# Kernel tuning notes

Measured on AMD Instinct MI355X. Metric: run time of the kernel, lower is better.

Reference implementation:

```python
import jax, jax.numpy as jnp
import numpy as np

N_EMBED = 1024
NUM_HEADS = 16
HEAD_SIZE = 64  # NUM_HEADS * HEAD_SIZE == N_EMBED
BLOCK_SIZE = 2048


def setup_inputs() -> dict:
    key = jax.random.key(0)
    ks = jax.random.split(key, 9)
    s = 1.0 / np.sqrt(N_EMBED)
    batch_x = jax.random.normal(ks[0], (4, BLOCK_SIZE, N_EMBED), dtype=jnp.float32)
    # stacked per-head linear params: weight [H, E, d], bias [H, d]
    Wq = jax.random.uniform(ks[1], (NUM_HEADS, N_EMBED, HEAD_SIZE), jnp.float32, -s, s)
    Wk = jax.random.uniform(ks[2], (NUM_HEADS, N_EMBED, HEAD_SIZE), jnp.float32, -s, s)
    Wv = jax.random.uniform(ks[3], (NUM_HEADS, N_EMBED, HEAD_SIZE), jnp.float32, -s, s)
    bq = jax.random.uniform(ks[4], (NUM_HEADS, HEAD_SIZE), jnp.float32, -s, s)
    bk = jax.random.uniform(ks[5], (NUM_HEADS, HEAD_SIZE), jnp.float32, -s, s)
    bv = jax.random.uniform(ks[6], (NUM_HEADS, HEAD_SIZE), jnp.float32, -s, s)
    Wp = jax.random.uniform(ks[7], (N_EMBED, N_EMBED), jnp.float32, -s, s)
    bp = jax.random.uniform(ks[8], (N_EMBED,), jnp.float32, -s, s)
    return {"batch_x": batch_x, "Wq": Wq, "Wk": Wk, "Wv": Wv,
            "bq": bq, "bk": bk, "bv": bv, "Wp": Wp, "bp": bp}


def reference(batch_x, Wq, Wk, Wv, bq, bk, bv, Wp, bp):
    B, T, E = batch_x.shape
    # per-head projections: [B, H, T, d]
    q = jnp.einsum('bte,hed->bhtd', batch_x, Wq) + bq[None, :, None, :]
    k = jnp.einsum('bte,hed->bhtd', batch_x, Wk) + bk[None, :, None, :]
    v = jnp.einsum('bte,hed->bhtd', batch_x, Wv) + bv[None, :, None, :]
    scale = 1.0 / jnp.sqrt(jnp.asarray(HEAD_SIZE, batch_x.dtype))
    wei = jnp.einsum('bhtd,bhsd->bhts', q, k) * scale  # [B,H,T,T]
    causal = jnp.tril(jnp.ones((T, T), dtype=bool))
    wei = jnp.where(causal, wei, jnp.asarray(-jnp.inf, wei.dtype))
    wei = jax.nn.softmax(wei, axis=-1)
    out = jnp.einsum('bhts,bhsd->bhtd', wei, v)  # [B,H,T,d]
    # concat heads (head order matches torch.cat over ModuleList)
    out = out.transpose(0, 2, 1, 3).reshape(B, T, NUM_HEADS * HEAD_SIZE)
    return out @ Wp + bp
```

## Files before the change

kernel.cpp:

```cpp
#include <hip/hip_runtime.h>
#include <math.h>

#define B_ 4
#define T_ 2048
#define E_ 1024
#define H_ 16
#define D_ 64

typedef __bf16 bf16_t;
typedef bf16_t bf16x8 __attribute__((ext_vector_type(8)));
typedef float  f32x4  __attribute__((ext_vector_type(4)));
typedef float  f32x16 __attribute__((ext_vector_type(16)));
typedef unsigned short u16x4 __attribute__((ext_vector_type(4)));
typedef unsigned int   u32x4 __attribute__((ext_vector_type(4)));

static __device__ __forceinline__ unsigned short f2bf(float f) {
    bf16_t h = (bf16_t)f;
    return __builtin_bit_cast(unsigned short, h);
}
static __device__ __forceinline__ unsigned int pk2(float a, float b) {
    return (unsigned int)f2bf(a) | ((unsigned int)f2bf(b) << 16);
}
static __device__ __forceinline__ float ex2(float x) {
    float r; asm("v_exp_f32 %0, %1" : "=v"(r) : "v"(x)); return r;
}
static __device__ __forceinline__ void pl32swap(unsigned int& a, unsigned int& b) {
    asm("v_permlane32_swap_b32 %0, %1" : "+v"(a), "+v"(b));
}

#define GLD(gp, lp) __builtin_amdgcn_global_load_lds( \
    (const __attribute__((address_space(1))) unsigned int*)(gp), \
    (__attribute__((address_space(3))) unsigned int*)(lp), 16, 0, 0)

#define BAR() __builtin_amdgcn_s_barrier()
#define WAIT_LGKM0() asm volatile("s_waitcnt lgkmcnt(0)" ::: "memory")
#define VMC(n) asm volatile("s_waitcnt vmcnt(" #n ")" ::: "memory")

__global__ void cast_x_kernel(const float* __restrict__ in, unsigned short* __restrict__ out, int n4) {
    int i = blockIdx.x * blockDim.x + threadIdx.x;
    if (i >= n4) return;
    float4 v = ((const float4*)in)[i];
    ushort4 o;
    o.x = f2bf(v.x); o.y = f2bf(v.y); o.z = f2bf(v.z); o.w = f2bf(v.w);
    ((ushort4*)out)[i] = o;
}

__global__ void tcast_all(const float* __restrict__ Wq, const float* __restrict__ Wk,
                          const float* __restrict__ Wv, const float* __restrict__ Wp,
                          unsigned short* __restrict__ wf, unsigned short* __restrict__ wpt) {
    __shared__ unsigned short Ts[64 * 66];
    const int grp = blockIdx.y >> 4, yy = blockIdx.y & 15;
    const float* in; unsigned short* out; int yA, S;
    if (grp == 3) { in = Wp; out = wpt; yA = 64;    S = 1024; }
    else {
        in = (grp == 0) ? Wq : (grp == 1) ? Wk : Wv;
        out = wf + (size_t)grp * 1024 * 1024; yA = 65536; S = 64;
    }
    const int tid = threadIdx.x;
    const int r = tid >> 2, c4 = tid & 3;
    const float* ip = in + (size_t)yA * yy + (size_t)(blockIdx.x * 64 + r) * S + c4 * 16;
    #pragma unroll
    for (int j = 0; j < 4; ++j) {
        float4 v = *(const float4*)&ip[j * 4];
        Ts[(c4 * 16 + j * 4 + 0) * 66 + r] = f2bf(v.x);
        Ts[(c4 * 16 + j * 4 + 1) * 66 + r] = f2bf(v.y);
        Ts[(c4 * 16 + j * 4 + 2) * 66 + r] = f2bf(v.z);
        Ts[(c4 * 16 + j * 4 + 3) * 66 + r] = f2bf(v.w);
    }
    __syncthreads();
    unsigned short* op = out + (size_t)(yy * 64 + r) * 1024 + blockIdx.x * 64 + c4 * 16;
    #pragma unroll
    for (int j = 0; j < 4; ++j) {
        u16x4 pk;
        #pragma unroll
        for (int m = 0; m < 4; ++m) pk[m] = Ts[r * 66 + c4 * 16 + j * 4 + m];
        *(u16x4*)&op[j * 4] = pk;
    }
}


#define GEMM_CORE_DECLS \
    const int tid = threadIdx.x; \
    const int w = tid >> 6, lane = tid & 63; \
    const int wr = w >> 2, wc = w & 3; \
    const int l15 = lane & 15, quad = lane >> 4, lsw = l15 & 7; \
    const int rowg = lane >> 3; \
    const int swz = ((lane & 7) ^ rowg) * 8; \
    f32x4 acc[4][4]; \
    _Pragma("unroll") for (int i_ = 0; i_ < 4; ++i_) \
        _Pragma("unroll") for (int j_ = 0; j_ < 4; ++j_) \
            acc[i_][j_] = (f32x4){0.f, 0.f, 0.f, 0.f};

#define MFMA_P(nb) \
    __builtin_amdgcn_s_setprio(1); \
    _Pragma("unroll") for (int m_ = 0; m_ < 4; ++m_) \
        _Pragma("unroll") for (int j_ = 0; j_ < 2; ++j_) \
            _Pragma("unroll") for (int k_ = 0; k_ < 2; ++k_) \
                acc[m_][(nb) + j_] = __builtin_amdgcn_mfma_f32_16x16x32_bf16( \
                    fA[m_][k_], fB[(nb) + j_][k_], acc[m_][(nb) + j_], 0, 0, 0); \
    __builtin_amdgcn_s_setprio(0);

#define GEMM_K_LOOP \
    stageA(0, 0); stageA(0, 1); stageB(0, 0, 0); stageB(0, 0, 1); \
    stageB(0, 1, 0); stageB(0, 1, 1); \
    stageA(1, 0); stageA(1, 1); stageB(1, 0, 0); stageB(1, 0, 1); \
    VMC(6); BAR(); \
    _Pragma("unroll 1") \
    for (int it = 0; it < 8; ++it) { \
        const int t0 = 2 * it, t1 = 2 * it + 1; \
        const bool more = it < 7; \
        bf16x8 fA[4][2], fB[4][2]; \
         \
        _Pragma("unroll") for (int m_ = 0; m_ < 4; ++m_) { fA[m_][0] = rdA(t0, m_, 0); fA[m_][1] = rdA(t0, m_, 1); } \
        _Pragma("unroll") for (int n_ = 0; n_ < 2; ++n_) { fB[n_][0] = rdB(t0, n_, 0); fB[n_][1] = rdB(t0, n_, 1); } \
        stageB(t1, 1, 0); stageB(t1, 1, 1); \
        BAR(); WAIT_LGKM0(); \
        MFMA_P(0); \
        VMC(6); BAR(); \
         \
        _Pragma("unroll") for (int n_ = 0; n_ < 2; ++n_) { fB[2 + n_][0] = rdB(t0, 2 + n_, 0); fB[2 + n_][1] = rdB(t0, 2 + n_, 1); } \
        if (more) { stageA(t0 + 2, 0); stageA(t0 + 2, 1); stageB(t0 + 2, 0, 0); stageB(t0 + 2, 0, 1); } \
        BAR(); WAIT_LGKM0(); \
        MFMA_P(2); \
        if (more) { VMC(6); } else { VMC(2); } \
        BAR(); \
         \
        _Pragma("unroll") for (int m_ = 0; m_ < 4; ++m_) { fA[m_][0] = rdA(t1, m_, 0); fA[m_][1] = rdA(t1, m_, 1); } \
        _Pragma("unroll") for (int n_ = 0; n_ < 2; ++n_) { fB[n_][0] = rdB(t1, n_, 0); fB[n_][1] = rdB(t1, n_, 1); } \
        if (more) { stageB(t0 + 2, 1, 0); stageB(t0 + 2, 1, 1); } \
        BAR(); WAIT_LGKM0(); \
        MFMA_P(0); \
        if (more) { VMC(6); } else { VMC(0); } \
        BAR(); \
         \
        _Pragma("unroll") for (int n_ = 0; n_ < 2; ++n_) { fB[2 + n_][0] = rdB(t1, 2 + n_, 0); fB[2 + n_][1] = rdB(t1, 2 + n_, 1); } \
        if (more) { stageA(t1 + 2, 0); stageA(t1 + 2, 1); stageB(t1 + 2, 0, 0); stageB(t1 + 2, 0, 1); } \
        BAR(); WAIT_LGKM0(); \
        MFMA_P(2); \
        if (more) { VMC(6); } \
        BAR(); \
    }

__global__ __launch_bounds__(512, 2) void qkv_gemm(
    const unsigned short* __restrict__ xb,
    const unsigned short* __restrict__ wf,
    const float* __restrict__ bq, const float* __restrict__ bk, const float* __restrict__ bv,
    unsigned short* __restrict__ qo, unsigned short* __restrict__ ko,
    unsigned short* __restrict__ vt)
{
    __shared__ __align__(16) unsigned short sm[49152];

    const int bid = blockIdx.x;
    const int m0 = (bid & 63) * 128;
    const int n0 = (bid >> 6) * 256;

    GEMM_CORE_DECLS

    auto stageA = [&](int t, int g) {
        const int rb = w * 16 + g * 8;
        unsigned short* dst = sm + (t & 1) * 24576 + rb * 64;
        GLD(xb + (size_t)(m0 + rb + rowg) * 1024 + t * 64 + swz, dst);
    };
    auto stageB = [&](int t, int R, int g) {
        const int rb = w * 16 + g * 8;
        const int ar0 = (rb >> 5) * 64 + R * 32 + (rb & 31);
        unsigned short* dst = sm + (t & 1) * 24576 + 8192 + ar0 * 64;
        GLD(wf + (size_t)(n0 + ar0 + rowg) * 1024 + t * 64 + swz, dst);
    };
    auto rdA = [&](int t, int fm, int ks) {
        const int row = wr * 64 + fm * 16 + l15;
        return *(const bf16x8*)&sm[(t & 1) * 24576 + row * 64 + (((ks * 4 + quad) ^ lsw) * 8)];
    };
    auto rdB = [&](int t, int fn, int ks) {
        const int row = wc * 64 + fn * 16 + l15;
        return *(const bf16x8*)&sm[(t & 1) * 24576 + 8192 + row * 64 + (((ks * 4 + quad) ^ lsw) * 8)];
    };

    GEMM_K_LOOP

    const int which = n0 >> 10;
    const int nb = n0 & 1023;
    if (which < 2) {
        const float* bias = which ? bk : bq;
        unsigned short* outp = which ? ko : qo;
        const float sc = which ? 1.f : 0.125f * 1.44269504088896f;
        #pragma unroll
        for (int fm = 0; fm < 4; ++fm)
            #pragma unroll
            for (int fn = 0; fn < 4; ++fn) {
                int colg = nb + wc * 64 + fn * 16 + l15;
                int h = colg >> 6, d = colg & 63;
                float bi = bias[colg];
                #pragma unroll
                for (int r = 0; r < 4; ++r) {
                    int row = m0 + wr * 64 + fm * 16 + quad * 4 + r;
                    int b = row >> 11, t = row & 2047;
                    outp[(((size_t)b * 16 + h) * 2048 + t) * 64 + d] = f2bf((acc[fm][fn][r] + bi) * sc);
                }
            }
    } else {
        const int b = m0 >> 11, t0r = m0 & 2047;
        for (int nh = 0; nh < 2; ++nh) {
            __syncthreads();
            if ((wc >> 1) == nh) {
                const int cc = wc & 1;
                #pragma unroll
                for (int fm = 0; fm < 4; ++fm)
                    #pragma unroll
                    for (int fn = 0; fn < 4; ++fn) {
                        int colL = cc * 64 + fn * 16 + l15;
                        int colg = nb + nh * 128 + colL;
                        float bi = bv[colg];
                        u16x4 pk;
                        #pragma unroll
                        for (int r = 0; r < 4; ++r) pk[r] = f2bf(acc[fm][fn][r] + bi);
                        *(u16x4*)&sm[colL * 136 + wr * 64 + fm * 16 + quad * 4] = pk;
                    }
            }
            __syncthreads();
            const int nl = tid >> 2, tq = tid & 3;
            const int colg = nb + nh * 128 + nl;
            const int h = colg >> 6, d = colg & 63;
            unsigned short* dst = vt + (((size_t)b * 16 + h) * 64 + d) * 2048 + t0r + tq * 32;
            #pragma unroll
            for (int j = 0; j < 4; ++j)
                *(float4*)&dst[j * 8] = *(const float4*)&sm[nl * 136 + tq * 32 + j * 8];
        }
    }
}

__global__ __launch_bounds__(512, 2) void proj_gemm(
    const unsigned short* __restrict__ A,
    const unsigned short* __restrict__ wpt,
    const float* __restrict__ bp,
    float* __restrict__ out)
{
    __shared__ __align__(16) unsigned short sm[49152];

    const int bid = blockIdx.x;
    const int m0 = (bid & 63) * 128;
    const int n0 = (bid >> 6) * 256;

    GEMM_CORE_DECLS

    const unsigned short* Ab = A + (size_t)(m0 >> 11) * 16 * 131072 + (size_t)(m0 & 2047) * 64;
    auto stageA = [&](int t, int g) {
        const int rb = w * 16 + g * 8;
        unsigned short* dst = sm + (t & 1) * 24576 + rb * 64;
        GLD(Ab + (size_t)t * 131072 + (rb + rowg) * 64 + swz, dst);
    };
    auto stageB = [&](int t, int R, int g) {
        const int rb = w * 16 + g * 8;
        const int ar0 = (rb >> 5) * 64 + R * 32 + (rb & 31);
        unsigned short* dst = sm + (t & 1) * 24576 + 8192 + ar0 * 64;
        GLD(wpt + (size_t)(n0 + ar0 + rowg) * 1024 + t * 64 + swz, dst);
    };
    auto rdA = [&](int t, int fm, int ks) {
        const int row = wr * 64 + fm * 16 + l15;
        return *(const bf16x8*)&sm[(t & 1) * 24576 + row * 64 + (((ks * 4 + quad) ^ lsw) * 8)];
    };
    auto rdB = [&](int t, int fn, int ks) {
        const int row = wc * 64 + fn * 16 + l15;
        return *(const bf16x8*)&sm[(t & 1) * 24576 + 8192 + row * 64 + (((ks * 4 + quad) ^ lsw) * 8)];
    };

    GEMM_K_LOOP

    #pragma unroll
    for (int fm = 0; fm < 4; ++fm)
        #pragma unroll
        for (int fn = 0; fn < 4; ++fn) {
            int col = n0 + wc * 64 + fn * 16 + l15;
            float bi = bp[col];
            #pragma unroll
            for (int r = 0; r < 4; ++r) {
                int row = m0 + wr * 64 + fm * 16 + quad * 4 + r;
                out[(size_t)row * 1024 + col] = acc[fm][fn][r] + bi;
            }
        }
}

__global__ __launch_bounds__(256, 2) void attn_kernel(
    const unsigned short* __restrict__ q, const unsigned short* __restrict__ k,
    const unsigned short* __restrict__ vt, unsigned short* __restrict__ att2)
{
    __shared__ __align__(16) unsigned short KV[2][2][8192];

    const int tid = threadIdx.x;
    const int w = tid >> 6, lane = tid & 63;
    const int l31 = lane & 31, h = lane >> 5;
    const int bh = blockIdx.x;
    const int rs = l31 & 7, rv = l31 & 15;

    const unsigned short* kb = k  + (size_t)bh * 2048 * 64;
    const unsigned short* vb = vt + (size_t)bh * 64 * 2048;

    const size_t kOff = (size_t)(32 * w + (lane >> 3)) * 64 + (size_t)(((lane & 7) ^ (lane >> 3)) * 8);
    const int vRow = lane >> 4, vc = lane & 15;
    size_t vOff[4];
    #pragma unroll
    for (int r = 0; r < 4; ++r)
        vOff[r] = (size_t)(16 * w + 4 * r + vRow) * 2048
                + (size_t)((vc ^ ((4 * r + vRow) & 15)) * 8);

    auto stage = [&](int jt, int buf) {
        unsigned short* dK = &KV[buf][0][w * 2048];
        unsigned short* dV = &KV[buf][1][w * 2048];
        const unsigned short* sK = kb + kOff + (size_t)jt * 8192;
        #pragma unroll
        for (int r = 0; r < 4; ++r) GLD(sK + r * 512, dK + r * 512);
        #pragma unroll
        for (int r = 0; r < 4; ++r) GLD(vb + vOff[r] + jt * 128, dV + r * 512);
    };

    for (int leg = 0; leg < 2; ++leg) {
        const int qtile = leg ? (15 - (int)blockIdx.y) : (int)blockIdx.y;
        const int qb0 = qtile * 128;
        const int qmin = qb0 + w * 32, qmax = qmin + 31;
        const int qg = qmin + l31;
        const int trips = qtile + 1;

        bf16x8 fQ[4];
        {
            const unsigned short* qp = q + ((size_t)bh * 2048 + qg) * 64 + h * 8;
            #pragma unroll
            for (int ks = 0; ks < 4; ++ks) fQ[ks] = *(const bf16x8*)&qp[ks * 16];
        }

        f32x16 Oa[2], Ob[2];
        #pragma unroll
        for (int nt = 0; nt < 2; ++nt)
            #pragma unroll
            for (int i = 0; i < 16; ++i) { Oa[nt][i] = 0.f; Ob[nt][i] = 0.f; }
        float lsum = 0.f;

        stage(0, 0);
        VMC(0);
        BAR();

        for (int jt = 0; jt < trips; ++jt) {
            const int buf = jt & 1;
            if (jt + 1 < trips) stage(jt + 1, buf ^ 1);
            const unsigned short* Ks = KV[buf][0];
            const unsigned short* Vs = KV[buf][1];
            const int key0 = jt * 128;

            f32x16 S[4];
            #pragma unroll
            for (int kt = 0; kt < 4; ++kt)
                #pragma unroll
                for (int i = 0; i < 16; ++i) S[kt][i] = 0.f;
            __builtin_amdgcn_s_setprio(1);
            #pragma unroll
            for (int kt = 0; kt < 4; ++kt) {
                if (key0 + 32 * kt <= qmax) {
                    const int row = kt * 32 + l31;
                    #pragma unroll
                    for (int ks = 0; ks < 4; ++ks) {
                        bf16x8 aK = *(const bf16x8*)&Ks[row * 64 + (((2 * ks + h) ^ rs) * 8)];
                        S[kt] = __builtin_amdgcn_mfma_f32_32x32x16_bf16(aK, fQ[ks], S[kt], 0, 0, 0);
                    }
                }
            }
            __builtin_amdgcn_s_setprio(0);

            #pragma unroll
            for (int kt = 0; kt < 4; ++kt) {
                if (key0 + 32 * kt <= qmax) {
                    const bool nm = (key0 + 32 * kt + 31) > qmin;
                    unsigned int e0[4], e1[4];
                    float lst = 0.f;
                    #pragma unroll
                    for (int g = 0; g < 4; ++g) {
                        float p[4];
                        #pragma unroll
                        for (int r = 0; r < 4; ++r) {
                            float pv = ex2(S[kt][4 * g + r]);
                            if (nm) {
                                int key = key0 + kt * 32 + 8 * g + 4 * h + r;
                                if (key > qg) pv = 0.f;
                            }
                            p[r] = pv;
                        }
                        lst += (p[0] + p[1]) + (p[2] + p[3]);
                        e0[g] = pk2(p[0], p[1]);
                        e1[g] = pk2(p[2], p[3]);
                    }
                    lsum += lst;

                    __builtin_amdgcn_s_setprio(1);
                    #pragma unroll
                    for (int s = 0; s < 2; ++s) {
                        unsigned int a = e0[2 * s], b = e0[2 * s + 1];
                        pl32swap(a, b);
                        unsigned int c2 = e1[2 * s], d2 = e1[2 * s + 1];
                        pl32swap(c2, d2);
                        u32x4 t; t[0] = a; t[1] = c2; t[2] = b; t[3] = d2;
                        bf16x8 aP = __builtin_bit_cast(bf16x8, t);
                        const int cb = 4 * kt + 2 * s;
                        #pragma unroll
                        for (int nt = 0; nt < 2; ++nt) {
                            const int drow = nt * 32 + l31;
                            bf16x8 bV = *(const bf16x8*)&Vs[drow * 128 + (((cb + h) ^ rv) * 8)];
                            if (kt & 1)
                                Ob[nt] = __builtin_amdgcn_mfma_f32_32x32x16_bf16(aP, bV, Ob[nt], 0, 0, 0);
                            else
                                Oa[nt] = __builtin_amdgcn_mfma_f32_32x32x16_bf16(aP, bV, Oa[nt], 0, 0, 0);
                        }
                    }
                    __builtin_amdgcn_s_setprio(0);
                }
            }

            VMC(0);
            BAR();
        }

        lsum += __shfl_xor(lsum, 32);
        const float inv = 1.f / lsum;

        unsigned short* ob = att2 + ((size_t)bh * 2048 + qmin) * 64;
        #pragma unroll
        for (int g = 0; g < 4; ++g)
            #pragma unroll
            for (int r = 0; r < 4; ++r) {
                const int qy = 8 * g + 4 * h + r;
                const float iv = __shfl(inv, qy);
                #pragma unroll
                for (int nt = 0; nt < 2; ++nt)
                    ob[(size_t)qy * 64 + nt * 32 + l31] =
                        f2bf((Oa[nt][4 * g + r] + Ob[nt][4 * g + r]) * iv);
            }
    }
}

extern "C" void kernel_launch(void* const* d_in, const int* in_sizes, int n_in,
                              void* d_out, int out_size, void* d_ws, size_t ws_size,
                              hipStream_t stream) {
    const float* x  = (const float*)d_in[0];
    const float* Wq = (const float*)d_in[1];
    const float* Wk = (const float*)d_in[2];
    const float* Wv = (const float*)d_in[3];
    const float* bq = (const float*)d_in[4];
    const float* bk = (const float*)d_in[5];
    const float* bv = (const float*)d_in[6];
    const float* Wp = (const float*)d_in[7];
    const float* bp = (const float*)d_in[8];
    float* out = (float*)d_out;

    const size_t nx = (size_t)B_ * T_ * E_;
    unsigned short* base = (unsigned short*)d_ws;
    unsigned short* xb  = base;
    unsigned short* qb  = xb + nx;
    unsigned short* kb  = qb + nx;
    unsigned short* vtb = kb + nx;
    unsigned short* atb = vtb + nx;
    unsigned short* wf  = atb + nx;
    unsigned short* wpt = wf + 3072 * 1024;

    cast_x_kernel<<<(int)(nx / 4 + 255) / 256, 256, 0, stream>>>(x, xb, (int)(nx / 4));
    tcast_all<<<dim3(16, 64), 256, 0, stream>>>(Wq, Wk, Wv, Wp, wf, wpt);
    qkv_gemm<<<768, 512, 0, stream>>>(xb, wf, bq, bk, bv, qb, kb, vtb);
    attn_kernel<<<dim3(64, 8), 256, 0, stream>>>(qb, kb, vtb, atb);
    proj_gemm<<<256, 512, 0, stream>>>(atb, wpt, bp, out);
}
```

Measured before the change: 255.1 us.

## Split attention key tiles across wave pairs and compute row sums via MFMA

Doubles the attention block to 8 waves, with each pair of waves sharing a 32-query group and splitting the 128-key tile into two halves. Partial outputs are merged through shared memory at the end of each leg. The softmax denominator is now produced by an extra MFMA against a vector of ones instead of scalar adds and shuffles. The aim is more waves per CU for latency hiding and shorter per-wave work, at the cost of an extra reduction pass, extra barriers and one additional MFMA per P-tile.

```diff
diff --git a/kernel.cpp b/kernel.cpp
--- a/kernel.cpp
+++ b/kernel.cpp
@@ -280,7 +280,7 @@
         }
 }
 
-__global__ __launch_bounds__(256, 2) void attn_kernel(
+__global__ __launch_bounds__(512, 4) void attn_kernel(
     const unsigned short* __restrict__ q, const unsigned short* __restrict__ k,
     const unsigned short* __restrict__ vt, unsigned short* __restrict__ att2)
 {
@@ -289,34 +289,39 @@
     const int tid = threadIdx.x;
     const int w = tid >> 6, lane = tid & 63;
     const int l31 = lane & 31, h = lane >> 5;
+    const int qg2 = w >> 1, ksel = w & 1;
     const int bh = blockIdx.x;
     const int rs = l31 & 7, rv = l31 & 15;
 
     const unsigned short* kb = k  + (size_t)bh * 2048 * 64;
     const unsigned short* vb = vt + (size_t)bh * 64 * 2048;
 
-    const size_t kOff = (size_t)(32 * w + (lane >> 3)) * 64 + (size_t)(((lane & 7) ^ (lane >> 3)) * 8);
+    u32x4 onesu; onesu[0] = onesu[1] = onesu[2] = onesu[3] = 0x3F803F80u;
+    const bf16x8 bOnes = __builtin_bit_cast(bf16x8, onesu);
+
+    const size_t kOff = (size_t)(16 * w + (lane >> 3)) * 64 + (size_t)(((lane & 7) ^ (lane >> 3)) * 8);
     const int vRow = lane >> 4, vc = lane & 15;
-    size_t vOff[4];
+    size_t vOff[2];
     #pragma unroll
-    for (int r = 0; r < 4; ++r)
-        vOff[r] = (size_t)(16 * w + 4 * r + vRow) * 2048
-                + (size_t)((vc ^ ((4 * r + vRow) & 15)) * 8);
+    for (int r = 0; r < 2; ++r) {
+        const int drow = 8 * w + 4 * r + vRow;
+        vOff[r] = (size_t)drow * 2048 + (size_t)((vc ^ (drow & 15)) * 8);
+    }
 
     auto stage = [&](int jt, int buf) {
-        unsigned short* dK = &KV[buf][0][w * 2048];
-        unsigned short* dV = &KV[buf][1][w * 2048];
+        unsigned short* dK = &KV[buf][0][w * 1024];
+        unsigned short* dV = &KV[buf][1][w * 1024];
         const unsigned short* sK = kb + kOff + (size_t)jt * 8192;
         #pragma unroll
-        for (int r = 0; r < 4; ++r) GLD(sK + r * 512, dK + r * 512);
-        #pragma unroll
-        for (int r = 0; r < 4; ++r) GLD(vb + vOff[r] + jt * 128, dV + r * 512);
+        for (int r = 0; r < 2; ++r) GLD(sK + r * 512, dK + r * 512);
+        #pragma unroll
+        for (int r = 0; r < 2; ++r) GLD(vb + vOff[r] + jt * 128, dV + r * 512);
     };
 
     for (int leg = 0; leg < 2; ++leg) {
         const int qtile = leg ? (15 - (int)blockIdx.y) : (int)blockIdx.y;
         const int qb0 = qtile * 128;
-        const int qmin = qb0 + w * 32, qmax = qmin + 31;
+        const int qmin = qb0 + qg2 * 32, qmax = qmin + 31;
         const int qg = qmin + l31;
         const int trips = qtile + 1;
 
@@ -327,12 +332,13 @@
             for (int ks = 0; ks < 4; ++ks) fQ[ks] = *(const bf16x8*)&qp[ks * 16];
         }
 
-        f32x16 Oa[2], Ob[2];
+        f32x16 O[2], Osum;
         #pragma unroll
         for (int nt = 0; nt < 2; ++nt)
             #pragma unroll
-            for (int i = 0; i < 16; ++i) { Oa[nt][i] = 0.f; Ob[nt][i] = 0.f; }
-        float lsum = 0.f;
+            for (int i = 0; i < 16; ++i) O[nt][i] = 0.f;
+        #pragma unroll
+        for (int i = 0; i < 16; ++i) Osum[i] = 0.f;
 
         stage(0, 0);
         VMC(0);
@@ -345,48 +351,47 @@
             const unsigned short* Vs = KV[buf][1];
             const int key0 = jt * 128;
 
-            f32x16 S[4];
-            #pragma unroll
-            for (int kt = 0; kt < 4; ++kt)
-                #pragma unroll
-                for (int i = 0; i < 16; ++i) S[kt][i] = 0.f;
+            f32x16 S[2];
+            #pragma unroll
+            for (int ktl = 0; ktl < 2; ++ktl)
+                #pragma unroll
+                for (int i = 0; i < 16; ++i) S[ktl][i] = 0.f;
             __builtin_amdgcn_s_setprio(1);
             #pragma unroll
-            for (int kt = 0; kt < 4; ++kt) {
-                if (key0 + 32 * kt <= qmax) {
-                    const int row = kt * 32 + l31;
+            for (int ktl = 0; ktl < 2; ++ktl) {
+                const int ktg = 2 * ksel + ktl;
+                if (key0 + 32 * ktg <= qmax) {
+                    const int row = ktg * 32 + l31;
                     #pragma unroll
                     for (int ks = 0; ks < 4; ++ks) {
                         bf16x8 aK = *(const bf16x8*)&Ks[row * 64 + (((2 * ks + h) ^ rs) * 8)];
-                        S[kt] = __builtin_amdgcn_mfma_f32_32x32x16_bf16(aK, fQ[ks], S[kt], 0, 0, 0);
+                        S[ktl] = __builtin_amdgcn_mfma_f32_32x32x16_bf16(aK, fQ[ks], S[ktl], 0, 0, 0);
                     }
                 }
             }
             __builtin_amdgcn_s_setprio(0);
 
             #pragma unroll
-            for (int kt = 0; kt < 4; ++kt) {
-                if (key0 + 32 * kt <= qmax) {
-                    const bool nm = (key0 + 32 * kt + 31) > qmin;
+            for (int ktl = 0; ktl < 2; ++ktl) {
+                const int ktg = 2 * ksel + ktl;
+                if (key0 + 32 * ktg <= qmax) {
+                    const bool nm = (key0 + 32 * ktg + 31) > qmin;
                     unsigned int e0[4], e1[4];
-                    float lst = 0.f;
                     #pragma unroll
                     for (int g = 0; g < 4; ++g) {
                         float p[4];
                         #pragma unroll
                         for (int r = 0; r < 4; ++r) {
-                            float pv = ex2(S[kt][4 * g + r]);
+                            float pv = ex2(S[ktl][4 * g + r]);
                             if (nm) {
-                                int key = key0 + kt * 32 + 8 * g + 4 * h + r;
+                                int key = key0 + ktg * 32 + 8 * g + 4 * h + r;
                                 if (key > qg) pv = 0.f;
                             }
                             p[r] = pv;
                         }
-                        lst += (p[0] + p[1]) + (p[2] + p[3]);
                         e0[g] = pk2(p[0], p[1]);
                         e1[g] = pk2(p[2], p[3]);
                     }
-                    lsum += lst;
 
                     __builtin_amdgcn_s_setprio(1);
                     #pragma unroll
@@ -397,16 +402,14 @@
                         pl32swap(c2, d2);
                         u32x4 t; t[0] = a; t[1] = c2; t[2] = b; t[3] = d2;
                         bf16x8 aP = __builtin_bit_cast(bf16x8, t);
-                        const int cb = 4 * kt + 2 * s;
+                        const int cb = 4 * ktg + 2 * s;
                         #pragma unroll
                         for (int nt = 0; nt < 2; ++nt) {
                             const int drow = nt * 32 + l31;
                             bf16x8 bV = *(const bf16x8*)&Vs[drow * 128 + (((cb + h) ^ rv) * 8)];
-                            if (kt & 1)
-                                Ob[nt] = __builtin_amdgcn_mfma_f32_32x32x16_bf16(aP, bV, Ob[nt], 0, 0, 0);
-                            else
-                                Oa[nt] = __builtin_amdgcn_mfma_f32_32x32x16_bf16(aP, bV, Oa[nt], 0, 0, 0);
+                            O[nt] = __builtin_amdgcn_mfma_f32_32x32x16_bf16(aP, bV, O[nt], 0, 0, 0);
                         }
+                        Osum = __builtin_amdgcn_mfma_f32_32x32x16_bf16(aP, bOnes, Osum, 0, 0, 0);
                     }
                     __builtin_amdgcn_s_setprio(0);
                 }
@@ -416,21 +419,43 @@
             BAR();
         }
 
-        lsum += __shfl_xor(lsum, 32);
-        const float inv = 1.f / lsum;
-
-        unsigned short* ob = att2 + ((size_t)bh * 2048 + qmin) * 64;
-        #pragma unroll
-        for (int g = 0; g < 4; ++g)
-            #pragma unroll
-            for (int r = 0; r < 4; ++r) {
-                const int qy = 8 * g + 4 * h + r;
-                const float iv = __shfl(inv, qy);
-                #pragma unroll
-                for (int nt = 0; nt < 2; ++nt)
-                    ob[(size_t)qy * 64 + nt * 32 + l31] =
-                        f2bf((Oa[nt][4 * g + r] + Ob[nt][4 * g + r]) * iv);
-            }
+        float* Lf = (float*)KV;
+        __syncthreads();
+        float* mb = Lf + (size_t)qg2 * 48 * 64;
+        if (ksel) {
+            #pragma unroll
+            for (int nt = 0; nt < 2; ++nt)
+                #pragma unroll
+                for (int i = 0; i < 16; ++i)
+                    mb[(nt * 16 + i) * 64 + lane] = O[nt][i];
+            #pragma unroll
+            for (int i = 0; i < 16; ++i)
+                mb[(32 + i) * 64 + lane] = Osum[i];
+        }
+        __syncthreads();
+        if (!ksel) {
+            #pragma unroll
+            for (int nt = 0; nt < 2; ++nt)
+                #pragma unroll
+                for (int i = 0; i < 16; ++i)
+                    O[nt][i] += mb[(nt * 16 + i) * 64 + lane];
+            #pragma unroll
+            for (int i = 0; i < 16; ++i)
+                Osum[i] += mb[(32 + i) * 64 + lane];
+
+            unsigned short* ob = att2 + ((size_t)bh * 2048 + qmin) * 64;
+            #pragma unroll
+            for (int g = 0; g < 4; ++g)
+                #pragma unroll
+                for (int r = 0; r < 4; ++r) {
+                    const float iv = 1.f / Osum[4 * g + r];
+                    const int qy = 8 * g + 4 * h + r;
+                    #pragma unroll
+                    for (int nt = 0; nt < 2; ++nt)
+                        ob[(size_t)qy * 64 + nt * 32 + l31] = f2bf(O[nt][4 * g + r] * iv);
+                }
+        }
+        __syncthreads();
     }
 }
 
@@ -461,6 +486,6 @@
     cast_x_kernel<<<(int)(nx / 4 + 255) / 256, 256, 0, stream>>>(x, xb, (int)(nx / 4));
     tcast_all<<<dim3(16, 64), 256, 0, stream>>>(Wq, Wk, Wv, Wp, wf, wpt);
     qkv_gemm<<<768, 512, 0, stream>>>(xb, wf, bq, bk, bv, qb, kb, vtb);
-    attn_kernel<<<dim3(64, 8), 256, 0, stream>>>(qb, kb, vtb, atb);
+    attn_kernel<<<dim3(64, 8), 512, 0, stream>>>(qb, kb, vtb, atb);
     proj_gemm<<<256, 512, 0, stream>>>(atb, wpt, bp, out);
 }
```

Measured after the change: 255.1 us. No clear change (+0.0%).
